# Kernel optimization log

Measured on AMD Instinct MI355X. Metric: run time of the kernel, lower is better.

The kernel has to match this reference:

```python
import jax, jax.numpy as jnp
import numpy as np
from jax import lax

D_MODEL = 512; N_HEADS = 32; HEAD_DIM = 16
D_INNER = 1024; D_STATE = 64; HDIM = 64; NH = 16; D_CONV = 4
CONV_CH = D_INNER + 2 * D_STATE          # 1152
D_INPROJ = 2 * D_INNER + 2 * D_STATE + NH  # 2192
B, L = 4, 1024


def setup_inputs() -> dict:
    key = jax.random.key(0)
    ks = jax.random.split(key, 16)
    def rn(k, shape, scale=0.02):
        return jax.random.normal(k, shape, jnp.float32) * scale
    inp = {"h": jax.random.normal(ks[0], (B, L, D_MODEL), jnp.float32)}
    inp["attn_in_w"] = rn(ks[1], (3 * D_MODEL, D_MODEL))
    inp["attn_in_b"] = jnp.zeros((3 * D_MODEL,), jnp.float32)
    inp["attn_out_w"] = rn(ks[2], (D_MODEL, D_MODEL))
    inp["attn_out_b"] = jnp.zeros((D_MODEL,), jnp.float32)
    i = 3
    for p in ("fwd", "bwd"):
        inp[f"{p}_inproj_w"] = rn(ks[i], (D_INPROJ, D_MODEL)); i += 1
        inp[f"{p}_conv_w"] = rn(ks[i], (CONV_CH, D_CONV), 0.1); i += 1
        inp[f"{p}_conv_b"] = jnp.zeros((CONV_CH,), jnp.float32)
        inp[f"{p}_dt_bias"] = rn(ks[i], (NH,), 0.5); i += 1
        inp[f"{p}_A_log"] = jnp.log(jax.random.uniform(ks[i], (NH,), jnp.float32, 1.0, 16.0)); i += 1
        inp[f"{p}_D"] = jnp.ones((NH,), jnp.float32)
        inp[f"{p}_norm_w"] = jnp.ones((D_INNER,), jnp.float32)
        inp[f"{p}_outproj_w"] = rn(ks[i], (D_MODEL, D_INNER)); i += 1
    inp["ln_w"] = jnp.ones((D_MODEL,), jnp.float32)
    inp["ln_b"] = jnp.zeros((D_MODEL,), jnp.float32)
    return inp


def _mha(h, in_w, in_b, out_w, out_b):
    b, l, d = h.shape
    qkv = h @ in_w.T + in_b
    q, k, v = jnp.split(qkv, 3, axis=-1)
    def heads(t):
        return t.reshape(b, l, N_HEADS, HEAD_DIM).transpose(0, 2, 1, 3)
    q, k, v = heads(q), heads(k), heads(v)
    scores = jnp.einsum('bhqd,bhkd->bhqk', q, k) * (1.0 / np.sqrt(HEAD_DIM))
    attn = jax.nn.softmax(scores, axis=-1)
    o = jnp.einsum('bhqk,bhkd->bhqd', attn, v).transpose(0, 2, 1, 3).reshape(b, l, d)
    return o @ out_w.T + out_b


def _causal_dwconv(x, w, bias):
    # x: (b, l, c), w: (c, k) depthwise causal conv
    xt = x.transpose(0, 2, 1)  # (b, c, l)
    out = lax.conv_general_dilated(xt, w[:, None, :], (1,), [(D_CONV - 1, 0)],
                                   feature_group_count=CONV_CH,
                                   dimension_numbers=('NCH', 'OIH', 'NCH'))
    return (out + bias[None, :, None]).transpose(0, 2, 1)


def _ssd(x, dt, A, Bm, Cm):
    # x: (b,l,nh,p), dt: (b,l,nh), Bm/Cm: (b,l,n) (ngroups=1)
    b = x.shape[0]
    dA = jnp.exp(dt * A)          # (b,l,nh)
    dtx = dt[..., None] * x       # (b,l,nh,p)
    def step(hst, inp):
        dA_t, dtx_t, B_t, C_t = inp
        hst = dA_t[:, :, None, None] * hst + dtx_t[..., None] * B_t[:, None, None, :]
        return hst, jnp.einsum('bhpn,bn->bhp', hst, C_t)
    init = jnp.zeros((b, NH, HDIM, D_STATE), x.dtype)
    _, ys = lax.scan(step, init, (dA.transpose(1, 0, 2), dtx.transpose(1, 0, 2, 3),
                                  Bm.transpose(1, 0, 2), Cm.transpose(1, 0, 2)))
    return ys.transpose(1, 0, 2, 3)  # (b,l,nh,p)


def _mamba2(u, inproj_w, conv_w, conv_b, dt_bias, A_log, Dp, norm_w, outproj_w):
    b, l, _ = u.shape
    zxbcdt = u @ inproj_w.T                      # (b,l,2192)
    z = zxbcdt[..., :D_INNER]
    xBC = zxbcdt[..., D_INNER:D_INNER + CONV_CH]
    dt = jax.nn.softplus(zxbcdt[..., D_INNER + CONV_CH:] + dt_bias)  # (b,l,nh)
    xBC = jax.nn.silu(_causal_dwconv(xBC, conv_w, conv_b))
    x = xBC[..., :D_INNER].reshape(b, l, NH, HDIM)
    Bm = xBC[..., D_INNER:D_INNER + D_STATE]
    Cm = xBC[..., D_INNER + D_STATE:]
    A = -jnp.exp(A_log)
    y = _ssd(x, dt, A, Bm, Cm) + Dp[None, None, :, None] * x
    y = y.reshape(b, l, D_INNER) * jax.nn.silu(z)  # gated (norm_before_gate=False)
    y = y * lax.rsqrt(jnp.mean(y * y, axis=-1, keepdims=True) + 1e-5) * norm_w  # RMSNormGated
    return y @ outproj_w.T


def reference(h, attn_in_w, attn_in_b, attn_out_w, attn_out_b,
              fwd_inproj_w, fwd_conv_w, fwd_conv_b, fwd_dt_bias, fwd_A_log, fwd_D, fwd_norm_w, fwd_outproj_w,
              bwd_inproj_w, bwd_conv_w, bwd_conv_b, bwd_dt_bias, bwd_A_log, bwd_D, bwd_norm_w, bwd_outproj_w,
              ln_w, ln_b):
    attn_out = _mha(h, attn_in_w, attn_in_b, attn_out_w, attn_out_b)
    fwd_out = _mamba2(h, fwd_inproj_w, fwd_conv_w, fwd_conv_b, fwd_dt_bias, fwd_A_log, fwd_D, fwd_norm_w, fwd_outproj_w)
    bwd_out = jnp.flip(_mamba2(jnp.flip(h, 1), bwd_inproj_w, bwd_conv_w, bwd_conv_b, bwd_dt_bias, bwd_A_log, bwd_D, bwd_norm_w, bwd_outproj_w), 1)
    s = h + attn_out + fwd_out + bwd_out
    mu = jnp.mean(s, axis=-1, keepdims=True)
    var = jnp.mean((s - mu) ** 2, axis=-1, keepdims=True)
    return (s - mu) * lax.rsqrt(var + 1e-5) * ln_w + ln_b
```

## Files before the change

kernel.cpp:

```cpp
#include <hip/hip_runtime.h>
#include <math.h>
#include <stdint.h>

#define B_ 4
#define L_ 1024
#define DM 512
#define NHA 32
#define HD 16
#define DI 1024
#define DSTATE 64
#define HDIM_ 64
#define NHM 16
#define DCONV 4
#define CONVCH 1152
#define DINPROJ 2192
#define NTOK (B_*L_)
#define QC 64
#define NC (L_/QC)
#define QKVS 5920

typedef __bf16 bf16x8 __attribute__((ext_vector_type(8)));
typedef float f32x4 __attribute__((ext_vector_type(4)));
typedef unsigned short ushort8 __attribute__((ext_vector_type(8)));
typedef unsigned short ushort4v __attribute__((ext_vector_type(4)));
typedef __fp16 fp16x2 __attribute__((ext_vector_type(2)));
typedef _Float16 f16x4 __attribute__((ext_vector_type(4)));
typedef _Float16 f16x8 __attribute__((ext_vector_type(8)));

__device__ __forceinline__ float siluf(float x) {
    return x / (1.0f + __expf(-x));
}

__device__ __forceinline__ unsigned short f2bf(float f) {
    unsigned u = __float_as_uint(f);
    unsigned r = (u + 0x7FFFu + ((u >> 16) & 1u)) >> 16;
    return (unsigned short)r;
}

__device__ __forceinline__ float bf2f(unsigned short u) {
    return __uint_as_float((unsigned)u << 16);
}

__device__ __forceinline__ void cvt8(const float* src, unsigned short* dst) {
    float4 a = ((const float4*)src)[0];
    float4 b = ((const float4*)src)[1];
    ushort8 o;
    o[0] = f2bf(a.x); o[1] = f2bf(a.y); o[2] = f2bf(a.z); o[3] = f2bf(a.w);
    o[4] = f2bf(b.x); o[5] = f2bf(b.y); o[6] = f2bf(b.z); o[7] = f2bf(b.w);
    *(ushort8*)dst = o;
}

__device__ __forceinline__ void gload16(const void* g, void* l) {
    auto gp = reinterpret_cast<const __attribute__((address_space(1))) unsigned int*>(
        reinterpret_cast<uintptr_t>(g));
    auto lp = reinterpret_cast<__attribute__((address_space(3))) unsigned int*>(
        reinterpret_cast<uintptr_t>(l));
    __builtin_amdgcn_global_load_lds(gp, lp, 16, 0, 0);
}

#define S0 262144
#define S1 (S0 + 98304)
#define S2 (S1 + 32768)
#define S3 (S2 + 140288)
#define S4 (S3 + 140288)
__global__ void cvt_all_kernel(const float* __restrict__ h, unsigned short* __restrict__ hB,
                               const float* __restrict__ w1, unsigned short* __restrict__ d1,
                               const float* __restrict__ w2, unsigned short* __restrict__ d2,
                               const float* __restrict__ w3, unsigned short* __restrict__ d3,
                               const float* __restrict__ w4, unsigned short* __restrict__ d4) {
    int i = blockIdx.x * blockDim.x + threadIdx.x;
    const float* src; unsigned short* dst; int off;
    if (i < S0)      { src = h;  dst = hB; off = i; }
    else if (i < S1) { src = w1; dst = d1; off = i - S0; }
    else if (i < S2) { src = w2; dst = d2; off = i - S1; }
    else if (i < S3) { src = w3; dst = d3; off = i - S2; }
    else             { src = w4; dst = d4; off = i - S3; }
    cvt8(src + (size_t)off * 8, dst + (size_t)off * 8);
}

__global__ void cvt_outproj_kernel(const float* __restrict__ fw, const float* __restrict__ bw,
                                   unsigned short* __restrict__ dst) {
    int i = blockIdx.x * blockDim.x + threadIdx.x;
    const int n8 = DM * DI / 8;
    int half = i >= n8;
    int off = half ? i - n8 : i;
    const float* src = half ? bw : fw;
    int e = off * 8;
    int r = e / DI, c = e % DI;
    cvt8(src + e, dst + (size_t)r * 2048 + half * 1024 + c);
}

template <int BN, bool OBF16, bool SWZ>
__global__ __launch_bounds__(256) void gemm_mfma_staged(
        const unsigned short* __restrict__ Ab, const unsigned short* __restrict__ Wb,
        const float* __restrict__ bias, int biasN, void* __restrict__ Cout,
        int M, int N, int K) {
    constexpr int BM = 128, BK = 32;
    constexpr int NF = BN / 32;
    constexpr int BLOADS = BN / 64;
    __shared__ unsigned short As[2][BM * BK];
    __shared__ unsigned short Bs[2][BN * BK];

    const int tid = threadIdx.x;
    const int wave = tid >> 6, lane = tid & 63;
    const int l15 = lane & 15, g = lane >> 4;
    const int wm = wave >> 1, wn = wave & 1;
    int m0, n0;
    if constexpr (SWZ) {
        int d = blockIdx.x;
        int xcd = d & 7, jj = d >> 3;
        n0 = (xcd * 6 + jj % 6) * BN;
        m0 = (jj / 6) * BM;
    } else {
        m0 = blockIdx.y * BM;
        n0 = blockIdx.x * BN;
    }

    f32x4 acc[4][NF];
    #pragma unroll
    for (int mi = 0; mi < 4; ++mi)
        #pragma unroll
        for (int nj = 0; nj < NF; ++nj) acc[mi][nj] = (f32x4){0.f, 0.f, 0.f, 0.f};

    auto stage = [&](int bufi, int k0) {
        #pragma unroll
        for (int i = 0; i < 2; ++i) {
            int c = (wave * 2 + i) * 64 + lane;
            int row = c >> 2;
            int kc = ((c & 3) ^ (row & 3)) * 8;
            gload16(Ab + (size_t)(m0 + row) * K + k0 + kc,
                    &As[bufi][(wave * 2 + i) * 64 * 8]);
        }
        #pragma unroll
        for (int i = 0; i < BLOADS; ++i) {
            int c = (wave * BLOADS + i) * 64 + lane;
            int row = c >> 2;
            int kc = ((c & 3) ^ (row & 3)) * 8;
            int rn = n0 + row; if (rn >= N) rn = N - 1;
            gload16(Wb + (size_t)rn * K + k0 + kc,
                    &Bs[bufi][(wave * BLOADS + i) * 64 * 8]);
        }
    };

    int cur = 0;
    stage(0, 0);
    __syncthreads();
    for (int k0 = 0; k0 < K; k0 += BK) {
        if (k0 + BK < K) stage(cur ^ 1, k0 + BK);
        const unsigned short* Ac = As[cur];
        const unsigned short* Bc = Bs[cur];
        bf16x8 af[4];
        #pragma unroll
        for (int mi = 0; mi < 4; ++mi) {
            int ar = wm * 64 + mi * 16 + l15;
            af[mi] = *(const bf16x8*)(Ac + ar * BK + ((g ^ (ar & 3)) * 8));
        }
        bf16x8 bfr[NF];
        #pragma unroll
        for (int nj = 0; nj < NF; ++nj) {
            int br = wn * (BN / 2) + nj * 16 + l15;
            bfr[nj] = *(const bf16x8*)(Bc + br * BK + ((g ^ (br & 3)) * 8));
        }
        #pragma unroll
        for (int mi = 0; mi < 4; ++mi)
            #pragma unroll
            for (int nj = 0; nj < NF; ++nj)
                acc[mi][nj] = __builtin_amdgcn_mfma_f32_16x16x32_bf16(af[mi], bfr[nj], acc[mi][nj], 0, 0, 0);
        __syncthreads();
        cur ^= 1;
    }

    #pragma unroll
    for (int mi = 0; mi < 4; ++mi) {
        int rbase = m0 + wm * 64 + mi * 16 + g * 4;
        #pragma unroll
        for (int nj = 0; nj < NF; ++nj) {
            int col = n0 + wn * (BN / 2) + nj * 16 + l15;
            if (col < N) {
                float bv = (bias && col < biasN) ? bias[col] : 0.f;
                #pragma unroll
                for (int r = 0; r < 4; ++r) {
                    float v = acc[mi][nj][r] + bv;
                    if constexpr (OBF16)
                        ((unsigned short*)Cout)[(size_t)(rbase + r) * N + col] = f2bf(v);
                    else
                        ((float*)Cout)[(size_t)(rbase + r) * N + col] = v;
                }
            }
        }
    }
}

#define KP 24
#define VP 132
__global__ __launch_bounds__(256) void attn_mfma_kernel(const unsigned short* __restrict__ qkv,
                                                        unsigned short* __restrict__ ob) {
    const int n = blockIdx.x;
    const int xcd = n & 7;
    const int j = n >> 3;
    const int bh = ((j >> 4) << 3) + xcd;
    const int qt = j & 15;
    const int h = bh & 31;
    const int b = bh >> 5;
    const int tid = threadIdx.x;
    const int wave = tid >> 6, lane = tid & 63;
    const int l15 = lane & 15, g = lane >> 4;

    __shared__ _Float16 Ksm[128 * KP];
    __shared__ _Float16 VsmT[16 * VP];

    const unsigned short* base = qkv + (size_t)b * L_ * QKVS;
    const int qrow = qt * 64 + wave * 16 + l15;

    f16x4 qf;
    {
        ushort4v qv = *(const ushort4v*)(base + (size_t)qrow * QKVS + h * 16 + g * 4);
        fp16x2 qa = __builtin_amdgcn_cvt_pkrtz(bf2f(qv[0]) * 0.25f, bf2f(qv[1]) * 0.25f);
        fp16x2 qb = __builtin_amdgcn_cvt_pkrtz(bf2f(qv[2]) * 0.25f, bf2f(qv[3]) * 0.25f);
        qf[0] = (_Float16)qa[0]; qf[1] = (_Float16)qa[1];
        qf[2] = (_Float16)qb[0]; qf[3] = (_Float16)qb[1];
    }
    f32x4 yacc = (f32x4){0.f, 0.f, 0.f, 0.f};
    float s = 0.f;

    const int sk = tid >> 1;
    const int sd = (tid & 1) * 8;

    for (int c0 = 0; c0 < L_; c0 += 128) {
        {
            ushort8 ka = *(const ushort8*)(base + (size_t)(c0 + sk) * QKVS + 512 + h * 16 + sd);
            fp16x2 k0 = __builtin_amdgcn_cvt_pkrtz(bf2f(ka[0]), bf2f(ka[1]));
            fp16x2 k1 = __builtin_amdgcn_cvt_pkrtz(bf2f(ka[2]), bf2f(ka[3]));
            fp16x2 k2 = __builtin_amdgcn_cvt_pkrtz(bf2f(ka[4]), bf2f(ka[5]));
            fp16x2 k3 = __builtin_amdgcn_cvt_pkrtz(bf2f(ka[6]), bf2f(ka[7]));
            f16x8 kv;
            kv[0] = (_Float16)k0[0]; kv[1] = (_Float16)k0[1];
            kv[2] = (_Float16)k1[0]; kv[3] = (_Float16)k1[1];
            kv[4] = (_Float16)k2[0]; kv[5] = (_Float16)k2[1];
            kv[6] = (_Float16)k3[0]; kv[7] = (_Float16)k3[1];
            *(f16x8*)(&Ksm[sk * KP + sd]) = kv;
            ushort8 va = *(const ushort8*)(base + (size_t)(c0 + sk) * QKVS + 1024 + h * 16 + sd);
            #pragma unroll
            for (int jj = 0; jj < 8; ++jj)
                VsmT[(sd + jj) * VP + sk] = (_Float16)bf2f(va[jj]);
        }
        __syncthreads();
        #pragma unroll
        for (int half = 0; half < 2; ++half) {
            f32x4 st[4];
            #pragma unroll
            for (int ks = 0; ks < 4; ++ks) {
                f16x4 kf = *(const f16x4*)(&Ksm[((half * 4 + ks) * 16 + l15) * KP + g * 4]);
                st[ks] = __builtin_amdgcn_mfma_f32_16x16x16f16(kf, qf, (f32x4){0.f,0.f,0.f,0.f}, 0, 0, 0);
            }
            float p[16];
            float cs = 0.f;
            #pragma unroll
            for (int ks = 0; ks < 4; ++ks) {
                #pragma unroll
                for (int r = 0; r < 4; ++r) {
                    p[ks * 4 + r] = __expf(st[ks][r]);
                    cs += p[ks * 4 + r];
                }
            }
            cs += __shfl_xor(cs, 16);
            cs += __shfl_xor(cs, 32);
            s += cs;
            #pragma unroll
            for (int ks = 0; ks < 4; ++ks) {
                fp16x2 plo = __builtin_amdgcn_cvt_pkrtz(p[ks*4+0], p[ks*4+1]);
                fp16x2 phi = __builtin_amdgcn_cvt_pkrtz(p[ks*4+2], p[ks*4+3]);
                f16x4 pf;
                pf[0] = (_Float16)plo[0]; pf[1] = (_Float16)plo[1];
                pf[2] = (_Float16)phi[0]; pf[3] = (_Float16)phi[1];
                f16x4 vf = *(const f16x4*)(&VsmT[l15 * VP + (half * 4 + ks) * 16 + g * 4]);
                yacc = __builtin_amdgcn_mfma_f32_16x16x16f16(vf, pf, yacc, 0, 0, 0);
            }
        }
        __syncthreads();
    }
    float inv = 1.f / s;
    ushort4v o;
    o[0] = f2bf(yacc[0] * inv);
    o[1] = f2bf(yacc[1] * inv);
    o[2] = f2bf(yacc[2] * inv);
    o[3] = f2bf(yacc[3] * inv);
    *(ushort4v*)(ob + (size_t)(b * L_ + qrow) * 512 + h * 16 + g * 4) = o;
}

__global__ void conv_silu_kernel(const unsigned short* __restrict__ megaA,
                                 const float* __restrict__ cw0, const float* __restrict__ cb0,
                                 const float* __restrict__ cw1, const float* __restrict__ cb1,
                                 unsigned short* __restrict__ out) {
    const int rev = blockIdx.y;
    const float* conv_w = rev ? cw1 : cw0;
    const float* conv_b = rev ? cb1 : cb0;
    int idx = blockIdx.x * blockDim.x + threadIdx.x;
    if (idx >= NTOK * (CONVCH / 4)) return;
    int c4 = (idx % (CONVCH / 4)) * 4;
    int bl = idx / (CONVCH / 4);
    int l = bl % L_;
    int b = bl / L_;
    const unsigned short* src = megaA + (size_t)b * L_ * QKVS + 1536 + rev * DINPROJ + 1024 + c4;
    float4 w0 = *(const float4*)(conv_w + (c4 + 0) * 4);
    float4 w1 = *(const float4*)(conv_w + (c4 + 1) * 4);
    float4 w2 = *(const float4*)(conv_w + (c4 + 2) * 4);
    float4 w3 = *(const float4*)(conv_w + (c4 + 3) * 4);
    float4 acc = *(const float4*)(conv_b + c4);
    const float wt[4][4] = {{w0.x, w0.y, w0.z, w0.w}, {w1.x, w1.y, w1.z, w1.w},
                            {w2.x, w2.y, w2.z, w2.w}, {w3.x, w3.y, w3.z, w3.w}};
    #pragma unroll
    for (int j = 0; j < 4; ++j) {
        int ll = rev ? (l + 3 - j) : (l - 3 + j);
        if (ll >= 0 && ll < L_) {
            ushort4v x = *(const ushort4v*)(src + (size_t)ll * QKVS);
            acc.x = fmaf(wt[0][j], bf2f(x[0]), acc.x);
            acc.y = fmaf(wt[1][j], bf2f(x[1]), acc.y);
            acc.z = fmaf(wt[2][j], bf2f(x[2]), acc.z);
            acc.w = fmaf(wt[3][j], bf2f(x[3]), acc.w);
        }
    }
    ushort4v o;
    o[0] = f2bf(siluf(acc.x)); o[1] = f2bf(siluf(acc.y));
    o[2] = f2bf(siluf(acc.z)); o[3] = f2bf(siluf(acc.w));
    *(ushort4v*)(out + (size_t)rev * NTOK * CONVCH + (size_t)bl * CONVCH + c4) = o;
}

__global__ void dt_exact_kernel(const float* __restrict__ h,
                                const float* __restrict__ wdt0, const float* __restrict__ bias0,
                                const float* __restrict__ wdt1, const float* __restrict__ bias1,
                                float* __restrict__ dt) {
    const int dir = blockIdx.y;
    const float* wdt = dir ? wdt1 : wdt0;
    const float* dbias = dir ? bias1 : bias0;
    const int row = blockIdx.x;
    const int tid = threadIdx.x;
    const int g = tid >> 4, j = tid & 15;
    const float* hr = h + (size_t)row * DM;
    const float* wr = wdt + (size_t)g * DM;
    float s = 0.f;
    #pragma unroll 8
    for (int t = 0; t < 32; ++t) {
        int k = j + t * 16;
        s = fmaf(hr[k], wr[k], s);
    }
    s += __shfl_xor(s, 1); s += __shfl_xor(s, 2);
    s += __shfl_xor(s, 4); s += __shfl_xor(s, 8);
    if (j == 0) {
        float v = s + dbias[g];
        dt[(size_t)dir * NTOK * NHM + (size_t)row * NHM + g] = (v > 20.f) ? v : log1pf(__expf(v));
    }
}

__global__ __launch_bounds__(256) void ssd_chunk_kernel(
        const unsigned short* __restrict__ xbcAll, const float* __restrict__ dtAll,
        const float* __restrict__ Al0, const float* __restrict__ Dp0,
        const float* __restrict__ Al1, const float* __restrict__ Dp1,
        unsigned short* __restrict__ y16, float* __restrict__ Sb0, float* __restrict__ Sb1,
        float* __restrict__ Edec) {
    const int dir = blockIdx.y;
    const int rev = dir;
    const unsigned short* xbc = xbcAll + (size_t)dir * NTOK * CONVCH;
    const float* dtb = dtAll + (size_t)dir * NTOK * NHM;
    float* Sbuf = dir ? Sb1 : Sb0;
    unsigned short* y = y16 + (size_t)dir * NTOK * DI;

    const int bid = blockIdx.x;
    const int q = bid & (NC - 1);
    const int bh = bid / NC;
    const int b = bh >> 4, h = bh & 15;
    const int tid = threadIdx.x;
    const int wave = tid >> 6, lane = tid & 63;
    const int l15 = lane & 15, l4 = lane >> 4;

    __shared__ unsigned short Bn[64 * 72];
    __shared__ unsigned short Cn[64 * 72];
    __shared__ unsigned short Btw[64 * 72];
    __shared__ unsigned short Gt[64 * 72];
    __shared__ unsigned short xT[64 * 72];
    __shared__ float sdt[QC], sc[QC], wsv[QC];

    const float A = -__expf((dir ? Al1 : Al0)[h]);
    const float Dh = (dir ? Dp1 : Dp0)[h];
    const int r = tid >> 2, qq = tid & 3;

    #pragma unroll
    for (int j = 0; j < 4; ++j) {
        int qd = qq + j * 4;
        int t = q * QC + r;
        int l = rev ? (L_ - 1 - t) : t;
        const unsigned short* rowp = xbc + (size_t)(b * L_ + l) * CONVCH;
        *(ushort4v*)&Bn[r * 72 + qd * 4] = *(const ushort4v*)(rowp + 1024 + qd * 4);
        *(ushort4v*)&Cn[r * 72 + qd * 4] = *(const ushort4v*)(rowp + 1088 + qd * 4);
    }
    if (tid < QC) {
        int t = q * QC + tid;
        int l = rev ? (L_ - 1 - t) : t;
        sdt[tid] = dtb[(size_t)(b * L_ + l) * NHM + h];
    }
    __syncthreads();
    if (tid == 0) {
        float run = 0.f;
        for (int i = 0; i < QC; ++i) { run += A * sdt[i]; sc[i] = run; }
    }
    __syncthreads();
    if (tid < QC) wsv[tid] = sdt[tid] * __expf(sc[QC - 1] - sc[tid]);
    if (tid == 0) Edec[dir * 1024 + bid] = __expf(sc[QC - 1]);
    __syncthreads();

    {
        int n = tid >> 2, s0 = (tid & 3) * 16;
        ushort8 o0, o1;
        #pragma unroll
        for (int k = 0; k < 8; ++k) {
            o0[k] = f2bf(bf2f(Bn[(s0 + k) * 72 + n]) * wsv[s0 + k]);
            o1[k] = f2bf(bf2f(Bn[(s0 + 8 + k) * 72 + n]) * wsv[s0 + 8 + k]);
        }
        *(ushort8*)&Btw[n * 72 + s0] = o0;
        *(ushort8*)&Btw[n * 72 + s0 + 8] = o1;
    }
    #pragma unroll
    for (int j = 0; j < 4; ++j) {
        int qd = qq + j * 4;
        int t = q * QC + r;
        int l = rev ? (L_ - 1 - t) : t;
        const unsigned short* rowp = xbc + (size_t)(b * L_ + l) * CONVCH + h * 64;
        ushort4v xv = *(const ushort4v*)(rowp + qd * 4);
        xT[(qd * 4 + 0) * 72 + r] = xv[0];
        xT[(qd * 4 + 1) * 72 + r] = xv[1];
        xT[(qd * 4 + 2) * 72 + r] = xv[2];
        xT[(qd * 4 + 3) * 72 + r] = xv[3];
    }
    __syncthreads();

    f32x4 accG[4];
    #pragma unroll
    for (int j = 0; j < 4; ++j) accG[j] = (f32x4){0.f, 0.f, 0.f, 0.f};
    #pragma unroll
    for (int k0 = 0; k0 < 64; k0 += 32) {
        bf16x8 af = *(const bf16x8*)&Bn[(wave * 16 + l15) * 72 + l4 * 8 + k0];
        #pragma unroll
        for (int j = 0; j < 4; ++j) {
            bf16x8 bfj = *(const bf16x8*)&Cn[(j * 16 + l15) * 72 + l4 * 8 + k0];
            accG[j] = __builtin_amdgcn_mfma_f32_16x16x32_bf16(af, bfj, accG[j], 0, 0, 0);
        }
    }
    #pragma unroll
    for (int j = 0; j < 4; ++j) {
        #pragma unroll
        for (int rr = 0; rr < 4; ++rr) {
            int s = wave * 16 + l4 * 4 + rr;
            int i = j * 16 + l15;
            float g = (s <= i) ? accG[j][rr] * sdt[s] * __expf(sc[i] - sc[s]) : 0.f;
            Gt[i * 72 + s] = f2bf(g);
        }
    }
    __syncthreads();

    {
        f32x4 accY[4];
        #pragma unroll
        for (int j = 0; j < 4; ++j) accY[j] = (f32x4){0.f, 0.f, 0.f, 0.f};
        #pragma unroll
        for (int k0 = 0; k0 < 64; k0 += 32) {
            bf16x8 af = *(const bf16x8*)&Gt[(wave * 16 + l15) * 72 + l4 * 8 + k0];
            #pragma unroll
            for (int j = 0; j < 4; ++j) {
                bf16x8 bfj = *(const bf16x8*)&xT[(j * 16 + l15) * 72 + l4 * 8 + k0];
                accY[j] = __builtin_amdgcn_mfma_f32_16x16x32_bf16(af, bfj, accY[j], 0, 0, 0);
            }
        }
        #pragma unroll
        for (int j = 0; j < 4; ++j) {
            #pragma unroll
            for (int rr = 0; rr < 4; ++rr) {
                int i = wave * 16 + l4 * 4 + rr;
                int p = j * 16 + l15;
                int t = q * QC + i;
                int l = rev ? (L_ - 1 - t) : t;
                float xv = bf2f(xT[p * 72 + i]);
                y[(size_t)(b * L_ + l) * DI + h * 64 + p] = f2bf(accY[j][rr] + Dh * xv);
            }
        }
    }
    {
        f32x4 accS[4];
        #pragma unroll
        for (int j = 0; j < 4; ++j) accS[j] = (f32x4){0.f, 0.f, 0.f, 0.f};
        #pragma unroll
        for (int k0 = 0; k0 < 64; k0 += 32) {
            bf16x8 af = *(const bf16x8*)&xT[(wave * 16 + l15) * 72 + l4 * 8 + k0];
            #pragma unroll
            for (int j = 0; j < 4; ++j) {
                bf16x8 bfj = *(const bf16x8*)&Btw[(j * 16 + l15) * 72 + l4 * 8 + k0];
                accS[j] = __builtin_amdgcn_mfma_f32_16x16x32_bf16(af, bfj, accS[j], 0, 0, 0);
            }
        }
        float* Sq = Sbuf + (size_t)bid * 4096;
        #pragma unroll
        for (int j = 0; j < 4; ++j) {
            #pragma unroll
            for (int rr = 0; rr < 4; ++rr) {
                int p = wave * 16 + l4 * 4 + rr;
                int n = j * 16 + l15;
                Sq[p * 64 + n] = accS[j][rr];
            }
        }
    }
}

__global__ void ssd_chain_kernel(float* __restrict__ Sb0, float* __restrict__ Sb1,
                                 const float* __restrict__ Edec) {
    const int dir = blockIdx.z;
    float* Sbuf = dir ? Sb1 : Sb0;
    const int bh = blockIdx.x;
    const int e = blockIdx.y * 256 + threadIdx.x;
    float* base = Sbuf + (size_t)bh * NC * 4096 + e;
    const float* Ep = Edec + dir * 1024 + bh * NC;
    float hst = 0.f;
    float tmp = base[0];
    #pragma unroll
    for (int q = 0; q < NC; ++q) {
        float nxt = (q + 1 < NC) ? base[(size_t)(q + 1) * 4096] : 0.f;
        float E = Ep[q];
        base[(size_t)q * 4096] = hst;
        hst = fmaf(E, hst, tmp);
        tmp = nxt;
    }
}

__global__ __launch_bounds__(256) void ssd_corr_kernel(
        const unsigned short* __restrict__ xbcAll, const float* __restrict__ dtAll,
        const float* __restrict__ Al0, const float* __restrict__ Al1,
        const float* __restrict__ Sb0, const float* __restrict__ Sb1,
        unsigned short* __restrict__ y16) {
    const int dir = blockIdx.y;
    const int rev = dir;
    const unsigned short* xbc = xbcAll + (size_t)dir * NTOK * CONVCH;
    const float* dtb = dtAll + (size_t)dir * NTOK * NHM;
    const float* Sbuf = dir ? Sb1 : Sb0;
    unsigned short* y = y16 + (size_t)dir * NTOK * DI;

    const int bid = blockIdx.x;
    const int q = bid & (NC - 1);
    const int bh = bid / NC;
    const int b = bh >> 4, h = bh & 15;
    const int tid = threadIdx.x;
    const int wave = tid >> 6, lane = tid & 63;
    const int l15 = lane & 15, l4 = lane >> 4;

    __shared__ unsigned short Cb[64 * 72];
    __shared__ unsigned short Hb[64 * 72];
    __shared__ float sdt[QC], sc[QC];
    const float A = -__expf((dir ? Al1 : Al0)[h]);
    const int r = tid >> 2, qq = tid & 3;
    const float* Sq = Sbuf + (size_t)bid * 4096;

    #pragma unroll
    for (int j = 0; j < 4; ++j) {
        int qd = qq + j * 4;
        int t = q * QC + r;
        int l = rev ? (L_ - 1 - t) : t;
        const unsigned short* rowp = xbc + (size_t)(b * L_ + l) * CONVCH;
        *(ushort4v*)&Cb[r * 72 + qd * 4] = *(const ushort4v*)(rowp + 1088 + qd * 4);
        float4 hv = ((const float4*)Sq)[r * 16 + qd];
        ushort4v hh;
        hh[0] = f2bf(hv.x); hh[1] = f2bf(hv.y); hh[2] = f2bf(hv.z); hh[3] = f2bf(hv.w);
        *(ushort4v*)&Hb[r * 72 + qd * 4] = hh;
    }
    if (tid < QC) {
        int t = q * QC + tid;
        int l = rev ? (L_ - 1 - t) : t;
        sdt[tid] = dtb[(size_t)(b * L_ + l) * NHM + h];
    }
    __syncthreads();
    if (tid == 0) {
        float run = 0.f;
        for (int i = 0; i < QC; ++i) { run += A * sdt[i]; sc[i] = run; }
    }
    __syncthreads();

    f32x4 acc[4];
    #pragma unroll
    for (int j = 0; j < 4; ++j) acc[j] = (f32x4){0.f, 0.f, 0.f, 0.f};
    #pragma unroll
    for (int k0 = 0; k0 < 64; k0 += 32) {
        bf16x8 af = *(const bf16x8*)&Cb[(wave * 16 + l15) * 72 + l4 * 8 + k0];
        #pragma unroll
        for (int j = 0; j < 4; ++j) {
            bf16x8 bfj = *(const bf16x8*)&Hb[(j * 16 + l15) * 72 + l4 * 8 + k0];
            acc[j] = __builtin_amdgcn_mfma_f32_16x16x32_bf16(af, bfj, acc[j], 0, 0, 0);
        }
    }
    #pragma unroll
    for (int j = 0; j < 4; ++j) {
        #pragma unroll
        for (int rr = 0; rr < 4; ++rr) {
            int i = wave * 16 + l4 * 4 + rr;
            int p = j * 16 + l15;
            int t = q * QC + i;
            int l = rev ? (L_ - 1 - t) : t;
            float e = __expf(sc[i]);
            unsigned short* yp = &y[(size_t)(b * L_ + l) * DI + h * 64 + p];
            *yp = f2bf(bf2f(*yp) + e * acc[j][rr]);
        }
    }
}

__global__ void gate_rmsnorm_kernel(const unsigned short* __restrict__ y16,
                                    const unsigned short* __restrict__ megaA,
                                    const float* __restrict__ nw0, const float* __restrict__ nw1,
                                    unsigned short* __restrict__ yb) {
    const int dir = blockIdx.y;
    const float* norm_w = dir ? nw1 : nw0;
    const int row = blockIdx.x;
    const int tid = threadIdx.x;
    const unsigned short* z = megaA + (size_t)row * QKVS + 1536 + dir * DINPROJ;
    const unsigned short* yr = y16 + (size_t)dir * NTOK * DI + (size_t)row * DI;
    float v[4];
    float ss = 0.f;
    #pragma unroll
    for (int i = 0; i < 4; ++i) {
        int c = i * 256 + tid;
        float g = siluf(bf2f(z[c]));
        v[i] = bf2f(yr[c]) * g;
        ss = fmaf(v[i], v[i], ss);
    }
    #pragma unroll
    for (int off = 32; off > 0; off >>= 1) ss += __shfl_xor(ss, off);
    __shared__ float red[4];
    int wid = tid >> 6, lane = tid & 63;
    if (lane == 0) red[wid] = ss;
    __syncthreads();
    ss = red[0] + red[1] + red[2] + red[3];
    float scale = rsqrtf(ss * (1.0f / 1024.0f) + 1e-5f);
    #pragma unroll
    for (int i = 0; i < 4; ++i) {
        int c = i * 256 + tid;
        yb[(size_t)row * 2048 + dir * 1024 + c] = f2bf(v[i] * scale * norm_w[c]);
    }
}

__global__ void final_ln_kernel(const float* __restrict__ h, const float* __restrict__ attn,
                                const float* __restrict__ msum,
                                const float* __restrict__ ln_w, const float* __restrict__ ln_b,
                                float* __restrict__ out) {
    const int row = blockIdx.x;
    const int tid = threadIdx.x;
    size_t base = (size_t)row * DM;
    float v[2];
    float sum = 0.f, sq = 0.f;
    #pragma unroll
    for (int i = 0; i < 2; ++i) {
        int c = i * 256 + tid;
        float s = h[base + c] + attn[base + c] + msum[base + c];
        v[i] = s;
        sum += s;
        sq = fmaf(s, s, sq);
    }
    #pragma unroll
    for (int off = 32; off > 0; off >>= 1) {
        sum += __shfl_xor(sum, off);
        sq += __shfl_xor(sq, off);
    }
    __shared__ float rsum[4], rsq[4];
    int wid = tid >> 6, lane = tid & 63;
    if (lane == 0) { rsum[wid] = sum; rsq[wid] = sq; }
    __syncthreads();
    sum = rsum[0] + rsum[1] + rsum[2] + rsum[3];
    sq = rsq[0] + rsq[1] + rsq[2] + rsq[3];
    float mu = sum * (1.0f / DM);
    float var = sq * (1.0f / DM) - mu * mu;
    float rs = rsqrtf(var + 1e-5f);
    #pragma unroll
    for (int i = 0; i < 2; ++i) {
        int c = i * 256 + tid;
        out[base + c] = (v[i] - mu) * rs * ln_w[c] + ln_b[c];
    }
}

extern "C" void kernel_launch(void* const* d_in, const int* in_sizes, int n_in,
                              void* d_out, int out_size, void* d_ws, size_t ws_size,
                              hipStream_t stream) {
    const float* h          = (const float*)d_in[0];
    const float* attn_in_w  = (const float*)d_in[1];
    const float* attn_in_b  = (const float*)d_in[2];
    const float* attn_out_w = (const float*)d_in[3];
    const float* attn_out_b = (const float*)d_in[4];
    const float* ln_w       = (const float*)d_in[21];
    const float* ln_b       = (const float*)d_in[22];
    float* out = (float*)d_out;

    float* ws = (float*)d_ws;
    unsigned short* megaA = (unsigned short*)ws;
    unsigned short* bufXBC = (unsigned short*)(ws + 12124160);
    float* bufDT   = ws + 12124160 + 4718592;
    float* bufY    = bufDT + 131072;
    float* bufATTN = bufY + 4194304;
    float* gateReg = bufATTN + 2097152;
    float* sReg    = gateReg + 4194304;
    float* bufEdec = sReg + 4194304;
    unsigned short* hB = (unsigned short*)(bufEdec + 2048);
    unsigned short* wBIG   = (unsigned short*)gateReg;
    unsigned short* wAOUT  = wBIG + (size_t)QKVS * DM;
    unsigned short* gatedB = (unsigned short*)gateReg;
    unsigned short* actB   = (unsigned short*)sReg;
    float* bufS0           = sReg;
    float* bufS1           = gateReg;
    unsigned short* wC     = (unsigned short*)sReg;
    unsigned short* y16    = (unsigned short*)bufY;
    float* msum            = bufY;

    const float* inproj_fwd = (const float*)d_in[5];
    const float* inproj_bwd = (const float*)d_in[13];

    dim3 blk(256);

    cvt_all_kernel<<<dim3(S4 / 256), blk, 0, stream>>>(
        h, hB, attn_in_w, wBIG, attn_out_w, wAOUT,
        inproj_fwd, wBIG + (size_t)1536 * DM, inproj_bwd, wBIG + (size_t)3728 * DM);

    gemm_mfma_staged<128, true, true><<<dim3(8 * 6 * (NTOK / 128)), blk, 0, stream>>>(
        hB, wBIG, attn_in_b, 1536, megaA, NTOK, QKVS, DM);

    attn_mfma_kernel<<<dim3(B_ * NHA * (L_ / 64)), blk, 0, stream>>>(megaA, actB);
    gemm_mfma_staged<64, false, false><<<dim3(DM / 64, NTOK / 128), blk, 0, stream>>>(
        actB, wAOUT, attn_out_b, DM, bufATTN, NTOK, DM, DM);

    dt_exact_kernel<<<dim3(NTOK, 2), blk, 0, stream>>>(
        h, inproj_fwd + (size_t)(DINPROJ - NHM) * DM, (const float*)d_in[8],
        inproj_bwd + (size_t)(DINPROJ - NHM) * DM, (const float*)d_in[16], bufDT);
    conv_silu_kernel<<<dim3((NTOK * (CONVCH / 4) + 255) / 256, 2), blk, 0, stream>>>(
        megaA, (const float*)d_in[6], (const float*)d_in[7],
        (const float*)d_in[14], (const float*)d_in[15], bufXBC);

    ssd_chunk_kernel<<<dim3(B_ * NHM * NC, 2), blk, 0, stream>>>(
        bufXBC, bufDT, (const float*)d_in[9], (const float*)d_in[10],
        (const float*)d_in[17], (const float*)d_in[18], y16, bufS0, bufS1, bufEdec);
    ssd_chain_kernel<<<dim3(B_ * NHM, 16, 2), blk, 0, stream>>>(bufS0, bufS1, bufEdec);
    ssd_corr_kernel<<<dim3(B_ * NHM * NC, 2), blk, 0, stream>>>(
        bufXBC, bufDT, (const float*)d_in[9], (const float*)d_in[17], bufS0, bufS1, y16);
    gate_rmsnorm_kernel<<<dim3(NTOK, 2), blk, 0, stream>>>(
        y16, megaA, (const float*)d_in[11], (const float*)d_in[19], gatedB);

    cvt_outproj_kernel<<<dim3((2 * DM * DI / 8 + 255) / 256), blk, 0, stream>>>(
        (const float*)d_in[12], (const float*)d_in[20], wC);
    gemm_mfma_staged<64, false, false><<<dim3(DM / 64, NTOK / 128), blk, 0, stream>>>(
        gatedB, wC, nullptr, 0, msum, NTOK, DM, 2048);

    final_ln_kernel<<<dim3(NTOK), blk, 0, stream>>>(
        h, bufATTN, msum, ln_w, ln_b, out);
}
```

Measured before the change: 238.9 us.

## Split-K out-projection GEMM, retile conv, fuse dt directions, tweak LDS swizzle

The out-projection GEMM (K=2048) is split into two K halves over blockIdx.z, writing separate partial buffers that the final LayerNorm sums, which doubles the block count. The LDS XOR swizzle changes to mix more row bits, and launch_bounds now requests 4 blocks per SM. The depthwise conv computes 4 consecutive tokens per thread from a 7-row window so loads are reused, and the dt kernel handles both directions in one block, sharing the h loads. Costs are an extra fp32 partial buffer written and read, and added register pressure.

After: 267.1 us. 1.12x slower.

```diff
diff --git a/kernel.cpp b/kernel.cpp
--- a/kernel.cpp
+++ b/kernel.cpp
@@ -56,6 +56,10 @@
     auto lp = reinterpret_cast<__attribute__((address_space(3))) unsigned int*>(
         reinterpret_cast<uintptr_t>(l));
     __builtin_amdgcn_global_load_lds(gp, lp, 16, 0, 0);
+}
+
+__device__ __forceinline__ int swz3(int row) {
+    return (row ^ (row >> 2)) & 3;
 }
 
 #define S0 262144
@@ -90,8 +94,8 @@
     cvt8(src + e, dst + (size_t)r * 2048 + half * 1024 + c);
 }
 
-template <int BN, bool OBF16, bool SWZ>
-__global__ __launch_bounds__(256) void gemm_mfma_staged(
+template <int BN, bool OBF16, bool SWZ, bool SPLITK>
+__global__ __launch_bounds__(256, 4) void gemm_mfma_staged(
         const unsigned short* __restrict__ Ab, const unsigned short* __restrict__ Wb,
         const float* __restrict__ bias, int biasN, void* __restrict__ Cout,
         int M, int N, int K) {
@@ -127,7 +131,7 @@
         for (int i = 0; i < 2; ++i) {
             int c = (wave * 2 + i) * 64 + lane;
             int row = c >> 2;
-            int kc = ((c & 3) ^ (row & 3)) * 8;
+            int kc = ((c & 3) ^ swz3(row)) * 8;
             gload16(Ab + (size_t)(m0 + row) * K + k0 + kc,
                     &As[bufi][(wave * 2 + i) * 64 * 8]);
         }
@@ -135,31 +139,34 @@
         for (int i = 0; i < BLOADS; ++i) {
             int c = (wave * BLOADS + i) * 64 + lane;
             int row = c >> 2;
-            int kc = ((c & 3) ^ (row & 3)) * 8;
+            int kc = ((c & 3) ^ swz3(row)) * 8;
             int rn = n0 + row; if (rn >= N) rn = N - 1;
             gload16(Wb + (size_t)rn * K + k0 + kc,
                     &Bs[bufi][(wave * BLOADS + i) * 64 * 8]);
         }
     };
 
+    const int kBeg = SPLITK ? blockIdx.z * (K >> 1) : 0;
+    const int kLen = SPLITK ? (K >> 1) : K;
+
     int cur = 0;
-    stage(0, 0);
-    __syncthreads();
-    for (int k0 = 0; k0 < K; k0 += BK) {
-        if (k0 + BK < K) stage(cur ^ 1, k0 + BK);
+    stage(0, kBeg);
+    __syncthreads();
+    for (int kk = 0; kk < kLen; kk += BK) {
+        if (kk + BK < kLen) stage(cur ^ 1, kBeg + kk + BK);
         const unsigned short* Ac = As[cur];
         const unsigned short* Bc = Bs[cur];
         bf16x8 af[4];
         #pragma unroll
         for (int mi = 0; mi < 4; ++mi) {
             int ar = wm * 64 + mi * 16 + l15;
-            af[mi] = *(const bf16x8*)(Ac + ar * BK + ((g ^ (ar & 3)) * 8));
+            af[mi] = *(const bf16x8*)(Ac + ar * BK + ((g ^ swz3(ar)) * 8));
         }
         bf16x8 bfr[NF];
         #pragma unroll
         for (int nj = 0; nj < NF; ++nj) {
             int br = wn * (BN / 2) + nj * 16 + l15;
-            bfr[nj] = *(const bf16x8*)(Bc + br * BK + ((g ^ (br & 3)) * 8));
+            bfr[nj] = *(const bf16x8*)(Bc + br * BK + ((g ^ swz3(br)) * 8));
         }
         #pragma unroll
         for (int mi = 0; mi < 4; ++mi)
@@ -170,6 +177,9 @@
         cur ^= 1;
     }
 
+    float* CoutF = (float*)Cout;
+    if constexpr (SPLITK) CoutF += (size_t)blockIdx.z * M * N;
+
     #pragma unroll
     for (int mi = 0; mi < 4; ++mi) {
         int rbase = m0 + wm * 64 + mi * 16 + g * 4;
@@ -177,14 +187,14 @@
         for (int nj = 0; nj < NF; ++nj) {
             int col = n0 + wn * (BN / 2) + nj * 16 + l15;
             if (col < N) {
-                float bv = (bias && col < biasN) ? bias[col] : 0.f;
+                float bv = (bias && col < biasN && (!SPLITK || blockIdx.z == 0)) ? bias[col] : 0.f;
                 #pragma unroll
                 for (int r = 0; r < 4; ++r) {
                     float v = acc[mi][nj][r] + bv;
                     if constexpr (OBF16)
                         ((unsigned short*)Cout)[(size_t)(rbase + r) * N + col] = f2bf(v);
                     else
-                        ((float*)Cout)[(size_t)(rbase + r) * N + col] = v;
+                        CoutF[(size_t)(rbase + r) * N + col] = v;
                 }
             }
         }
@@ -295,60 +305,81 @@
     const int rev = blockIdx.y;
     const float* conv_w = rev ? cw1 : cw0;
     const float* conv_b = rev ? cb1 : cb0;
+    const int NC4 = CONVCH / 4;
     int idx = blockIdx.x * blockDim.x + threadIdx.x;
-    if (idx >= NTOK * (CONVCH / 4)) return;
-    int c4 = (idx % (CONVCH / 4)) * 4;
-    int bl = idx / (CONVCH / 4);
-    int l = bl % L_;
-    int b = bl / L_;
+    if (idx >= (NTOK / 4) * NC4) return;
+    int c4 = (idx % NC4) * 4;
+    int lt = idx / NC4;
+    int l0 = (lt & (L_ / 4 - 1)) * 4;
+    int b = lt / (L_ / 4);
     const unsigned short* src = megaA + (size_t)b * L_ * QKVS + 1536 + rev * DINPROJ + 1024 + c4;
+
+    const int wsrow = rev ? l0 : l0 - 3;
+    ushort4v x[7];
+    #pragma unroll
+    for (int i = 0; i < 7; ++i) {
+        int rr = wsrow + i;
+        if (rr >= 0 && rr < L_) {
+            x[i] = *(const ushort4v*)(src + (size_t)rr * QKVS);
+        } else {
+            x[i][0] = 0; x[i][1] = 0; x[i][2] = 0; x[i][3] = 0;
+        }
+    }
+
     float4 w0 = *(const float4*)(conv_w + (c4 + 0) * 4);
     float4 w1 = *(const float4*)(conv_w + (c4 + 1) * 4);
     float4 w2 = *(const float4*)(conv_w + (c4 + 2) * 4);
     float4 w3 = *(const float4*)(conv_w + (c4 + 3) * 4);
-    float4 acc = *(const float4*)(conv_b + c4);
+    float4 bias = *(const float4*)(conv_b + c4);
     const float wt[4][4] = {{w0.x, w0.y, w0.z, w0.w}, {w1.x, w1.y, w1.z, w1.w},
                             {w2.x, w2.y, w2.z, w2.w}, {w3.x, w3.y, w3.z, w3.w}};
-    #pragma unroll
-    for (int j = 0; j < 4; ++j) {
-        int ll = rev ? (l + 3 - j) : (l - 3 + j);
-        if (ll >= 0 && ll < L_) {
-            ushort4v x = *(const ushort4v*)(src + (size_t)ll * QKVS);
-            acc.x = fmaf(wt[0][j], bf2f(x[0]), acc.x);
-            acc.y = fmaf(wt[1][j], bf2f(x[1]), acc.y);
-            acc.z = fmaf(wt[2][j], bf2f(x[2]), acc.z);
-            acc.w = fmaf(wt[3][j], bf2f(x[3]), acc.w);
-        }
-    }
-    ushort4v o;
-    o[0] = f2bf(siluf(acc.x)); o[1] = f2bf(siluf(acc.y));
-    o[2] = f2bf(siluf(acc.z)); o[3] = f2bf(siluf(acc.w));
-    *(ushort4v*)(out + (size_t)rev * NTOK * CONVCH + (size_t)bl * CONVCH + c4) = o;
+
+    unsigned short* ob = out + (size_t)rev * NTOK * CONVCH + (size_t)(b * L_ + l0) * CONVCH + c4;
+    #pragma unroll
+    for (int jj = 0; jj < 4; ++jj) {
+        float4 acc = bias;
+        #pragma unroll
+        for (int j = 0; j < 4; ++j) {
+            int wi = rev ? (jj + 3 - j) : (jj + j);
+            acc.x = fmaf(wt[0][j], bf2f(x[wi][0]), acc.x);
+            acc.y = fmaf(wt[1][j], bf2f(x[wi][1]), acc.y);
+            acc.z = fmaf(wt[2][j], bf2f(x[wi][2]), acc.z);
+            acc.w = fmaf(wt[3][j], bf2f(x[wi][3]), acc.w);
+        }
+        ushort4v o;
+        o[0] = f2bf(siluf(acc.x)); o[1] = f2bf(siluf(acc.y));
+        o[2] = f2bf(siluf(acc.z)); o[3] = f2bf(siluf(acc.w));
+        *(ushort4v*)(ob + (size_t)jj * CONVCH) = o;
+    }
 }
 
 __global__ void dt_exact_kernel(const float* __restrict__ h,
                                 const float* __restrict__ wdt0, const float* __restrict__ bias0,
                                 const float* __restrict__ wdt1, const float* __restrict__ bias1,
                                 float* __restrict__ dt) {
-    const int dir = blockIdx.y;
-    const float* wdt = dir ? wdt1 : wdt0;
-    const float* dbias = dir ? bias1 : bias0;
     const int row = blockIdx.x;
     const int tid = threadIdx.x;
     const int g = tid >> 4, j = tid & 15;
     const float* hr = h + (size_t)row * DM;
-    const float* wr = wdt + (size_t)g * DM;
-    float s = 0.f;
+    const float* wr0 = wdt0 + (size_t)g * DM;
+    const float* wr1 = wdt1 + (size_t)g * DM;
+    float s0 = 0.f, s1 = 0.f;
     #pragma unroll 8
     for (int t = 0; t < 32; ++t) {
         int k = j + t * 16;
-        s = fmaf(hr[k], wr[k], s);
-    }
-    s += __shfl_xor(s, 1); s += __shfl_xor(s, 2);
-    s += __shfl_xor(s, 4); s += __shfl_xor(s, 8);
+        float hv = hr[k];
+        s0 = fmaf(hv, wr0[k], s0);
+        s1 = fmaf(hv, wr1[k], s1);
+    }
+    s0 += __shfl_xor(s0, 1); s0 += __shfl_xor(s0, 2);
+    s0 += __shfl_xor(s0, 4); s0 += __shfl_xor(s0, 8);
+    s1 += __shfl_xor(s1, 1); s1 += __shfl_xor(s1, 2);
+    s1 += __shfl_xor(s1, 4); s1 += __shfl_xor(s1, 8);
     if (j == 0) {
-        float v = s + dbias[g];
-        dt[(size_t)dir * NTOK * NHM + (size_t)row * NHM + g] = (v > 20.f) ? v : log1pf(__expf(v));
+        float v0 = s0 + bias0[g];
+        float v1 = s1 + bias1[g];
+        dt[(size_t)row * NHM + g] = (v0 > 20.f) ? v0 : log1pf(__expf(v0));
+        dt[(size_t)NTOK * NHM + (size_t)row * NHM + g] = (v1 > 20.f) ? v1 : log1pf(__expf(v1));
     }
 }
 
@@ -642,7 +673,7 @@
 }
 
 __global__ void final_ln_kernel(const float* __restrict__ h, const float* __restrict__ attn,
-                                const float* __restrict__ msum,
+                                const float* __restrict__ msum, const float* __restrict__ msum2,
                                 const float* __restrict__ ln_w, const float* __restrict__ ln_b,
                                 float* __restrict__ out) {
     const int row = blockIdx.x;
@@ -653,7 +684,7 @@
     #pragma unroll
     for (int i = 0; i < 2; ++i) {
         int c = i * 256 + tid;
-        float s = h[base + c] + attn[base + c] + msum[base + c];
+        float s = h[base + c] + attn[base + c] + msum[base + c] + msum2[base + c];
         v[i] = s;
         sum += s;
         sq = fmaf(s, s, sq);
@@ -710,6 +741,7 @@
     unsigned short* wC     = (unsigned short*)sReg;
     unsigned short* y16    = (unsigned short*)bufY;
     float* msum            = bufY;
+    float* msum2           = bufY + (size_t)NTOK * DM;
 
     const float* inproj_fwd = (const float*)d_in[5];
     const float* inproj_bwd = (const float*)d_in[13];
@@ -720,17 +752,17 @@
         h, hB, attn_in_w, wBIG, attn_out_w, wAOUT,
         inproj_fwd, wBIG + (size_t)1536 * DM, inproj_bwd, wBIG + (size_t)3728 * DM);
 
-    gemm_mfma_staged<128, true, true><<<dim3(8 * 6 * (NTOK / 128)), blk, 0, stream>>>(
+    gemm_mfma_staged<128, true, true, false><<<dim3(8 * 6 * (NTOK / 128)), blk, 0, stream>>>(
         hB, wBIG, attn_in_b, 1536, megaA, NTOK, QKVS, DM);
 
     attn_mfma_kernel<<<dim3(B_ * NHA * (L_ / 64)), blk, 0, stream>>>(megaA, actB);
-    gemm_mfma_staged<64, false, false><<<dim3(DM / 64, NTOK / 128), blk, 0, stream>>>(
+    gemm_mfma_staged<64, false, false, false><<<dim3(DM / 64, NTOK / 128), blk, 0, stream>>>(
         actB, wAOUT, attn_out_b, DM, bufATTN, NTOK, DM, DM);
 
-    dt_exact_kernel<<<dim3(NTOK, 2), blk, 0, stream>>>(
+    dt_exact_kernel<<<dim3(NTOK), blk, 0, stream>>>(
         h, inproj_fwd + (size_t)(DINPROJ - NHM) * DM, (const float*)d_in[8],
         inproj_bwd + (size_t)(DINPROJ - NHM) * DM, (const float*)d_in[16], bufDT);
-    conv_silu_kernel<<<dim3((NTOK * (CONVCH / 4) + 255) / 256, 2), blk, 0, stream>>>(
+    conv_silu_kernel<<<dim3(((NTOK / 4) * (CONVCH / 4) + 255) / 256, 2), blk, 0, stream>>>(
         megaA, (const float*)d_in[6], (const float*)d_in[7],
         (const float*)d_in[14], (const float*)d_in[15], bufXBC);
 
@@ -745,9 +777,9 @@
 
     cvt_outproj_kernel<<<dim3((2 * DM * DI / 8 + 255) / 256), blk, 0, stream>>>(
         (const float*)d_in[12], (const float*)d_in[20], wC);
-    gemm_mfma_staged<64, false, false><<<dim3(DM / 64, NTOK / 128), blk, 0, stream>>>(
+    gemm_mfma_staged<64, false, false, true><<<dim3(DM / 64, NTOK / 128, 2), blk, 0, stream>>>(
         gatedB, wC, nullptr, 0, msum, NTOK, DM, 2048);
 
     final_ln_kernel<<<dim3(NTOK), blk, 0, stream>>>(
-        h, bufATTN, msum, ln_w, ln_b, out);
-}
+        h, bufATTN, msum, msum2, ln_w, ln_b, out);
+}
```
